# Performance work log

Measured on AMD Instinct MI355X. Metric: run time of the kernel, lower is better.

## Reference

```python
import jax, jax.numpy as jnp
import numpy as np

N_NODES = 50000
N_EDGES = 100000
N_GRAPHS = 2000
F_IN = 32      # num_node_features
EF = 16        # num_edge_features (unpacked bits)
H = 32         # hidden_dim
H2 = 64        # hidden_dim * 2


def _lin(key, fan_in, fan_out):
    kw, kb = jax.random.split(key)
    scale = 1.0 / np.sqrt(fan_in)
    W = jax.random.uniform(kw, (fan_in, fan_out), jnp.float32, -scale, scale)
    b = jax.random.uniform(kb, (fan_out,), jnp.float32, -scale, scale)
    return W, b


def setup_inputs() -> dict:
    key = jax.random.key(0)
    ks = jax.random.split(key, 16)
    x = jax.random.normal(ks[0], (N_NODES, F_IN), jnp.float32)
    edge_index = jax.random.randint(ks[1], (2, N_EDGES), 0, N_NODES, jnp.int64)
    edge_attr_packed = jax.random.randint(ks[2], (N_EDGES, 2), 0, 256, jnp.int32)
    batch = jnp.sort(jax.random.randint(ks[3], (N_NODES,), 0, N_GRAPHS, jnp.int64))

    W1a, b1a = _lin(ks[4], EF, H * F_IN)
    W1b, b1b = _lin(ks[5], H * F_IN, H * F_IN)
    W2a, b2a = _lin(ks[6], EF, H * H)
    W2b, b2b = _lin(ks[7], H * H, H * H * 2)
    root1 = jax.random.normal(ks[8], (F_IN, H), jnp.float32) / np.sqrt(F_IN)
    bias1 = jnp.zeros((H,), jnp.float32)
    root2 = jax.random.normal(ks[9], (H, H2), jnp.float32) / np.sqrt(H)
    bias2 = jnp.zeros((H2,), jnp.float32)
    fcW1, fcb1 = _lin(ks[10], H2, 512)
    fcW2, fcb2 = _lin(ks[11], 512, 512)
    fcW3, fcb3 = _lin(ks[12], 512, 256)
    fcW4, fcb4 = _lin(ks[13], 256, 3)
    return dict(x=x, edge_index=edge_index, edge_attr_packed=edge_attr_packed, batch=batch,
                W1a=W1a, b1a=b1a, W1b=W1b, b1b=b1b, W2a=W2a, b2a=b2a, W2b=W2b, b2b=b2b,
                root1=root1, bias1=bias1, root2=root2, bias2=bias2,
                fcW1=fcW1, fcb1=fcb1, fcW2=fcW2, fcb2=fcb2,
                fcW3=fcW3, fcb3=fcb3, fcW4=fcW4, fcb4=fcb4)


def _unpack_bits(ea_packed):
    # MSB-first bit unpack of each byte, matching torch f_unpackbits(mask=1)
    shifts = jnp.arange(7, -1, -1, dtype=jnp.int32)          # [8]
    bits = (ea_packed[:, :, None] >> shifts) & 1             # [E, W, 8]
    return bits.reshape(ea_packed.shape[0], -1).astype(jnp.float32)  # [E, W*8]


def _seg_mean(vals, idx, n):
    s = jax.ops.segment_sum(vals, idx, num_segments=n)
    c = jax.ops.segment_sum(jnp.ones((vals.shape[0], 1), vals.dtype), idx, num_segments=n)
    return s / jnp.maximum(c, 1.0)


def _nnconv(x, src, dst, theta, root, bias, f_in, f_out):
    # theta: [E, f_in*f_out] -> per-edge weight matrices (PyG view(-1, in, out))
    Wm = theta.reshape(-1, f_in, f_out)
    msg = jnp.einsum('ei,eio->eo', x[src], Wm)               # per-edge matmul
    agg = _seg_mean(msg, dst, x.shape[0])                    # scatter-mean at targets
    return agg + x @ root + bias


def reference(x, edge_index, edge_attr_packed, batch,
              W1a, b1a, W1b, b1b, W2a, b2a, W2b, b2b,
              root1, bias1, root2, bias2,
              fcW1, fcb1, fcW2, fcb2, fcW3, fcb3, fcW4, fcb4):
    relu = jax.nn.relu
    ea = _unpack_bits(edge_attr_packed)                      # [E, 16]
    src, dst = edge_index[0], edge_index[1]

    theta1 = relu(ea @ W1a + b1a) @ W1b + b1b                # [E, H*F_IN]
    h = relu(_nnconv(x, src, dst, theta1, root1, bias1, F_IN, H))

    theta2 = relu(ea @ W2a + b2a) @ W2b + b2b                # [E, H*H2]
    h = relu(_nnconv(h, src, dst, theta2, root2, bias2, H, H2))

    g = _seg_mean(h, batch, N_GRAPHS)                        # global_mean_pool
    g = relu(g @ fcW1 + fcb1)
    g = relu(g @ fcW2 + fcb2)
    g = relu(g @ fcW3 + fcb3)
    return g @ fcW4 + fcb4
```

## Files before the change

### kernel.cpp

```cpp
#include <hip/hip_runtime.h>

#define E_N 100000
#define NV_N 50000
#define NG_N 2000

typedef short s8v __attribute__((ext_vector_type(8)));
typedef unsigned short u16x8 __attribute__((ext_vector_type(8)));
typedef unsigned int u32x4 __attribute__((ext_vector_type(4)));
typedef float f32x4 __attribute__((ext_vector_type(4)));

__device__ __forceinline__ float bf2f(unsigned short u) {
  return __uint_as_float(((unsigned int)u) << 16);
}
__device__ __forceinline__ unsigned short f2bf(float f) {
  unsigned int u = __float_as_uint(f);
  u = u + 0x7fffu + ((u >> 16) & 1u);
  return (unsigned short)(u >> 16);
}


__global__ void k_tables(const float* __restrict__ W1a, const float* __restrict__ b1a,
                         const float* __restrict__ W2a, const float* __restrict__ b2a,
                         unsigned short* __restrict__ tabs) {
  int tid = blockIdx.x * 256 + threadIdx.x;
  int tb = tid >> 18, v = (tid >> 10) & 255, k = tid & 1023;
  const float* W = (tb < 2) ? W1a : W2a;
  int rbase = (tb & 1) ? 8 : 0;
  float s = 0.f;
  if ((tb & 1) == 0) s = (tb < 2) ? b1a[k] : b2a[k];
  #pragma unroll
  for (int j = 0; j < 8; ++j)
    if ((v >> (7 - j)) & 1) s += W[(rbase + j) * 1024 + k];
  tabs[tid] = f2bf(s);
}

__global__ void k_pack(const float* __restrict__ src, unsigned short* __restrict__ dst, int N) {
  int tid = blockIdx.x * 256 + threadIdx.x;
  int total = (1024 / 8) * N;
  if (tid >= total) return;
  int fi = tid >> 6, r = tid & 63;
  int lg = r >> 4, ll = r & 15;
  int nf = fi & 1, ks = (fi >> 1) & 3;
  int rest = fi >> 3;
  int nc32 = N / 32;
  int cb = rest % nc32, q = rest / nc32;
  int k0 = q * 128 + ks * 32 + lg * 8;
  int n = cb * 32 + nf * 16 + ll;
  u16x8 v;
  #pragma unroll
  for (int u = 0; u < 8; ++u)
    v[u] = f2bf(src[(size_t)(k0 + u) * N + n]);
  *(u16x8*)&dst[(size_t)tid * 8] = v;
}

__global__ void k_count(const int* __restrict__ ei, int* __restrict__ cnt) {
  int e = blockIdx.x * 256 + threadIdx.x;
  if (e < E_N) atomicAdd(&cnt[ei[E_N + e]], 1);
}

template<int NCOLS, int FOUT>
__global__ void __launch_bounds__(256, 2)
k_edge(const float* __restrict__ xsrc, const int* __restrict__ ei,
       const int* __restrict__ eap,
       const unsigned short* __restrict__ tab0,
       const unsigned short* __restrict__ tab1,
       const unsigned short* __restrict__ WP,
       const float* __restrict__ bvec,
       float* __restrict__ agg)
{
  constexpr int NP = NCOLS / 64;

  __shared__ unsigned short sHid[128 * 128];
  __shared__ float sXT[32 * 132];
  __shared__ int sSrc[128], sDst[128];
  __shared__ unsigned char sb0[128], sb1[128];

  const int t = threadIdx.x;
  const int l = t & 63;
  const int wid = t >> 6;
  const int wr = wid >> 1;
  const int wc = wid & 1;
  const int lg = l >> 4;
  const int ll = l & 15;
  const int e0 = blockIdx.x * 128;

  auto build = [&](int q) {
    int m = t >> 1, half = t & 1;
    const unsigned short* p0 = tab0 + (size_t)sb0[m] * 1024 + q * 128 + half * 64;
    const unsigned short* p1 = tab1 + (size_t)sb1[m] * 1024 + q * 128 + half * 64;
    #pragma unroll
    for (int j = 0; j < 8; ++j) {
      u16x8 a = *(const u16x8*)(p0 + j * 8);
      u16x8 b = *(const u16x8*)(p1 + j * 8);
      u32x4 hw;
      #pragma unroll
      for (int p = 0; p < 4; ++p) {
        float f0 = fmaxf(bf2f(a[2 * p]) + bf2f(b[2 * p]), 0.f);
        float f1 = fmaxf(bf2f(a[2 * p + 1]) + bf2f(b[2 * p + 1]), 0.f);
        unsigned int r01;
        asm("v_cvt_pk_bf16_f32 %0, %1, %2" : "=v"(r01) : "v"(f0), "v"(f1));
        hw[p] = r01;
      }
      int kb = half * 8 + j;
      *(u32x4*)&sHid[m * 128 + 8 * (kb ^ (m & 15))] = hw;
    }
  };

  const unsigned short* bp[4];
  #pragma unroll
  for (int k = 0; k < 4; ++k)
    bp[k] = WP + (size_t)((wc * 4 + k) * 2) * 512 + (size_t)l * 8;

  s8v rb[4][2];
  #pragma unroll
  for (int k = 0; k < 4; ++k) {
    rb[k][0] = *(const s8v*)bp[k];
    rb[k][1] = *(const s8v*)(bp[k] + 512);
    bp[k] += 8192;
  }

  if (t < 128) {
    int e = e0 + t;
    if (e < E_N) {
      sSrc[t] = ei[e]; sDst[t] = ei[E_N + e];
      sb0[t] = (unsigned char)(eap[2 * e] & 255);
      sb1[t] = (unsigned char)(eap[2 * e + 1] & 255);
    } else { sSrc[t] = 0; sDst[t] = -1; sb0[t] = 0; sb1[t] = 0; }
  }
  __syncthreads();
  for (int j = t; j < 128 * 32; j += 256) {
    int m = j >> 5, i = j & 31;
    sXT[i * 132 + m] = (e0 + m < E_N) ? xsrc[(size_t)sSrc[m] * 32 + i] : 0.f;
  }
  build(0);
  __syncthreads();

  f32x4 msgr[4][2] = {};

  #pragma unroll 1
  for (int q = 0; q < 8; ++q) {
    if (q > 0) {
      __syncthreads();
      build(q);
      __syncthreads();
    }
    s8v av[4][4];
    #pragma unroll
    for (int mf = 0; mf < 4; ++mf) {
      int row = wr * 64 + mf * 16 + ll;
      #pragma unroll
      for (int ks = 0; ks < 4; ++ks) {
        int kb = ks * 4 + lg;
        av[mf][ks] = *(const s8v*)&sHid[row * 128 + 8 * (kb ^ (row & 15))];
        asm volatile("" : "+v"(av[mf][ks]));
      }
    }
    #pragma unroll 1
    for (int np = 0; np < NP; ++np) {
      f32x4 acc[4][2];
      __builtin_amdgcn_s_setprio(1);
      #pragma unroll
      for (int mf = 0; mf < 4; ++mf)
        #pragma unroll
        for (int nf = 0; nf < 2; ++nf)
          acc[mf][nf] = __builtin_amdgcn_mfma_f32_16x16x32_bf16(
              av[mf][0], rb[0][nf], (f32x4){0.f, 0.f, 0.f, 0.f}, 0, 0, 0);
      __builtin_amdgcn_s_setprio(0);
      rb[0][0] = *(const s8v*)bp[0];
      rb[0][1] = *(const s8v*)(bp[0] + 512);
      bp[0] += 8192;
      __builtin_amdgcn_s_setprio(1);
      #pragma unroll
      for (int mf = 0; mf < 4; ++mf)
        #pragma unroll
        for (int nf = 0; nf < 2; ++nf)
          acc[mf][nf] = __builtin_amdgcn_mfma_f32_16x16x32_bf16(
              av[mf][1], rb[1][nf], acc[mf][nf], 0, 0, 0);
      __builtin_amdgcn_s_setprio(0);
      rb[1][0] = *(const s8v*)bp[1];
      rb[1][1] = *(const s8v*)(bp[1] + 512);
      bp[1] += 8192;
      __builtin_amdgcn_s_setprio(1);
      #pragma unroll
      for (int mf = 0; mf < 4; ++mf)
        #pragma unroll
        for (int nf = 0; nf < 2; ++nf)
          acc[mf][nf] = __builtin_amdgcn_mfma_f32_16x16x32_bf16(
              av[mf][2], rb[2][nf], acc[mf][nf], 0, 0, 0);
      __builtin_amdgcn_s_setprio(0);
      rb[2][0] = *(const s8v*)bp[2];
      rb[2][1] = *(const s8v*)(bp[2] + 512);
      bp[2] += 8192;
      __builtin_amdgcn_s_setprio(1);
      #pragma unroll
      for (int mf = 0; mf < 4; ++mf)
        #pragma unroll
        for (int nf = 0; nf < 2; ++nf)
          acc[mf][nf] = __builtin_amdgcn_mfma_f32_16x16x32_bf16(
              av[mf][3], rb[3][nf], acc[mf][nf], 0, 0, 0);
      __builtin_amdgcn_s_setprio(0);
      rb[3][0] = *(const s8v*)bp[3];
      rb[3][1] = *(const s8v*)(bp[3] + 512);
      bp[3] += 8192;

      const int iidx = (FOUT == 64) ? np : np * 2 + wc;
      #pragma unroll
      for (int mf = 0; mf < 4; ++mf) {
        f32x4 xv = *(const f32x4*)&sXT[iidx * 132 + wr * 64 + mf * 16 + lg * 4];
        msgr[mf][0] += acc[mf][0] * xv;
        msgr[mf][1] += acc[mf][1] * xv;
      }
    }
  }

  #pragma unroll 4
  for (int i = 0; i < 32; ++i) {
    if (FOUT == 32 && (i & 1) != wc) continue;
    float w0, w1;
    {
      int ob = (FOUT == 64) ? wc * 32 : 0;
      w0 = bvec[i * FOUT + ob + ll];
      w1 = bvec[i * FOUT + ob + 16 + ll];
    }
    #pragma unroll
    for (int mf = 0; mf < 4; ++mf) {
      f32x4 xv = *(const f32x4*)&sXT[i * 132 + wr * 64 + mf * 16 + lg * 4];
      msgr[mf][0] += xv * w0;
      msgr[mf][1] += xv * w1;
    }
  }

  #pragma unroll
  for (int nf = 0; nf < 2; ++nf) {
    const int o = ((FOUT == 64) ? (wc * 2 + nf) * 16 : nf * 16) + ll;
    #pragma unroll
    for (int mf = 0; mf < 4; ++mf)
      #pragma unroll
      for (int r = 0; r < 4; ++r) {
        int row = wr * 64 + mf * 16 + lg * 4 + r;
        int d = sDst[row];
        if (d >= 0) atomicAdd(&agg[(size_t)d * FOUT + o], msgr[mf][nf][r]);
      }
  }
}


__global__ void k_node1(const float* __restrict__ x, const float* __restrict__ agg,
                        const int* __restrict__ cnt, const float* __restrict__ root,
                        const float* __restrict__ bias, float* __restrict__ h) {
  int tid = blockIdx.x * 256 + threadIdx.x;
  if (tid >= NV_N * 32) return;
  int n = tid >> 5, j = tid & 31;
  const float* xr = x + n * 32;
  float s = 0.f;
  #pragma unroll
  for (int i = 0; i < 32; ++i) s = fmaf(xr[i], root[i * 32 + j], s);
  int c = cnt[n]; if (c < 1) c = 1;
  h[tid] = fmaxf(agg[tid] / (float)c + s + bias[j], 0.f);
}

__global__ void k_node2(const float* __restrict__ hin, const float* __restrict__ agg,
                        const int* __restrict__ cnt, const float* __restrict__ root,
                        const float* __restrict__ bias, float* __restrict__ h2) {
  int tid = blockIdx.x * 256 + threadIdx.x;
  if (tid >= NV_N * 64) return;
  int n = tid >> 6, j = tid & 63;
  const float* xr = hin + n * 32;
  float s = 0.f;
  #pragma unroll
  for (int i = 0; i < 32; ++i) s = fmaf(xr[i], root[i * 64 + j], s);
  int c = cnt[n]; if (c < 1) c = 1;
  h2[tid] = fmaxf(agg[tid] / (float)c + s + bias[j], 0.f);
}

__device__ __forceinline__ int lowerb(const int* __restrict__ a, int n, int key) {
  int lo = 0, hi = n;
  while (lo < hi) { int mid = (lo + hi) >> 1; if (a[mid] < key) lo = mid + 1; else hi = mid; }
  return lo;
}

__global__ void k_pool(const float* __restrict__ h2, const int* __restrict__ batch,
                       float* __restrict__ g) {
  int gid = (blockIdx.x * 256 + threadIdx.x) >> 6;
  int l = threadIdx.x & 63;
  if (gid >= NG_N) return;
  int lo = lowerb(batch, NV_N, gid);
  int hi = lowerb(batch, NV_N, gid + 1);
  float s = 0.f;
  for (int n = lo; n < hi; ++n) s += h2[n * 64 + l];
  int c = hi - lo; if (c < 1) c = 1;
  g[gid * 64 + l] = s / (float)c;
}

template<int K, bool RELU>
__global__ void k_fc(const float* __restrict__ A, const float* __restrict__ W,
                     const float* __restrict__ bias, float* __restrict__ out, int N) {
  __shared__ float sA[8][K];
  int r0 = blockIdx.x * 8;
  int n = blockIdx.y * 256 + threadIdx.x;
  for (int j = threadIdx.x; j < 8 * K; j += 256) {
    int rr = j / K, kk = j - rr * K;
    int r = r0 + rr;
    sA[rr][kk] = (r < NG_N) ? A[r * K + kk] : 0.f;
  }
  __syncthreads();
  float acc[8] = {0.f, 0.f, 0.f, 0.f, 0.f, 0.f, 0.f, 0.f};
  for (int k = 0; k < K; ++k) {
    float b = W[k * N + n];
    #pragma unroll
    for (int rr = 0; rr < 8; ++rr) acc[rr] = fmaf(sA[rr][k], b, acc[rr]);
  }
  float bs = bias[n];
  #pragma unroll
  for (int rr = 0; rr < 8; ++rr) {
    int r = r0 + rr;
    if (r < NG_N) {
      float v = acc[rr] + bs;
      if (RELU) v = fmaxf(v, 0.f);
      out[r * N + n] = v;
    }
  }
}

__global__ void k_fc4(const float* __restrict__ A, const float* __restrict__ W,
                      const float* __restrict__ bias, float* __restrict__ out) {
  int tid = blockIdx.x * 256 + threadIdx.x;
  int r = tid >> 2, s = tid & 3;
  if (r >= NG_N || s >= 3) return;
  float acc = bias[s];
  for (int k = 0; k < 256; ++k) acc = fmaf(A[r * 256 + k], W[k * 3 + s], acc);
  out[r * 3 + s] = acc;
}


extern "C" void kernel_launch(void* const* d_in, const int* in_sizes, int n_in,
                              void* d_out, int out_size, void* d_ws, size_t ws_size,
                              hipStream_t stream) {
  const float* x     = (const float*)d_in[0];
  const int*   ei    = (const int*)d_in[1];
  const int*   eap   = (const int*)d_in[2];
  const int*   batch = (const int*)d_in[3];
  const float* W1a   = (const float*)d_in[4];
  const float* b1a   = (const float*)d_in[5];
  const float* W1b   = (const float*)d_in[6];
  const float* b1b   = (const float*)d_in[7];
  const float* W2a   = (const float*)d_in[8];
  const float* b2a   = (const float*)d_in[9];
  const float* W2b   = (const float*)d_in[10];
  const float* b2b   = (const float*)d_in[11];
  const float* root1 = (const float*)d_in[12];
  const float* bias1 = (const float*)d_in[13];
  const float* root2 = (const float*)d_in[14];
  const float* bias2 = (const float*)d_in[15];
  const float* fcW1  = (const float*)d_in[16];
  const float* fcb1  = (const float*)d_in[17];
  const float* fcW2  = (const float*)d_in[18];
  const float* fcb2  = (const float*)d_in[19];
  const float* fcW3  = (const float*)d_in[20];
  const float* fcb3  = (const float*)d_in[21];
  const float* fcW4  = (const float*)d_in[22];
  const float* fcb4  = (const float*)d_in[23];
  float* out = (float*)d_out;

  char* w = (char*)d_ws;
  size_t off = 0;
  auto take = [&](size_t bytes) -> void* {
    void* p = w + off;
    off = (off + bytes + 255) & ~(size_t)255;
    return p;
  };
  unsigned short* tabs = (unsigned short*)take(4 * 256 * 1024 * 2);
  unsigned short* w1p  = (unsigned short*)take((size_t)1024 * 1024 * 2 + 32768);
  unsigned short* w2p  = (unsigned short*)take((size_t)1024 * 2048 * 2 + 32768);
  float* agg1 = (float*)take((size_t)NV_N * 32 * 4);
  float* agg2 = (float*)take((size_t)NV_N * 64 * 4);
  int*   cnt  = (int*)take((size_t)NV_N * 4);
  float* h    = (float*)take((size_t)NV_N * 32 * 4);
  float* h2   = (float*)take((size_t)NV_N * 64 * 4);
  float* g    = (float*)take((size_t)NG_N * 64 * 4);
  float* l1   = (float*)take((size_t)NG_N * 512 * 4);
  float* l2   = (float*)take((size_t)NG_N * 512 * 4);
  float* l3   = (float*)take((size_t)NG_N * 256 * 4);

  hipMemsetAsync(agg1, 0, (size_t)NV_N * 32 * 4, stream);
  hipMemsetAsync(agg2, 0, (size_t)NV_N * 64 * 4, stream);
  hipMemsetAsync(cnt, 0, (size_t)NV_N * 4, stream);

  k_tables<<<4096, 256, 0, stream>>>(W1a, b1a, W2a, b2a, tabs);
  k_pack<<<(1024 * 1024 / 8 + 255) / 256, 256, 0, stream>>>(W1b, w1p, 1024);
  k_pack<<<(1024 * 2048 / 8 + 255) / 256, 256, 0, stream>>>(W2b, w2p, 2048);
  k_count<<<(E_N + 255) / 256, 256, 0, stream>>>(ei, cnt);

  const int nblk = (E_N + 127) / 128;
  k_edge<1024, 32><<<nblk, 256, 0, stream>>>(x, ei, eap, tabs, tabs + 262144,
                                             w1p, b1b, agg1);
  k_node1<<<(NV_N * 32) / 256, 256, 0, stream>>>(x, agg1, cnt, root1, bias1, h);

  k_edge<2048, 64><<<nblk, 256, 0, stream>>>(h, ei, eap, tabs + 2 * 262144, tabs + 3 * 262144,
                                             w2p, b2b, agg2);
  k_node2<<<(NV_N * 64) / 256, 256, 0, stream>>>(h, agg2, cnt, root2, bias2, h2);

  k_pool<<<(NG_N * 64) / 256, 256, 0, stream>>>(h2, batch, g);

  k_fc<64, true><<<dim3((NG_N + 7) / 8, 2), 256, 0, stream>>>(g, fcW1, fcb1, l1, 512);
  k_fc<512, true><<<dim3((NG_N + 7) / 8, 2), 256, 0, stream>>>(l1, fcW2, fcb2, l2, 512);
  k_fc<512, true><<<dim3((NG_N + 7) / 8, 1), 256, 0, stream>>>(l2, fcW3, fcb3, l3, 256);
  k_fc4<<<(NG_N * 4 + 255) / 256, 256, 0, stream>>>(l3, fcW4, fcb4, out);
}
```

Baseline: 811.9 us.

## Pre-gather source features into transposed global buffer instead of per-block LDS staging

Adds a separate gather kernel that writes source-node features per edge into a transposed [32, EP] global array. The edge kernel then reads x values straight from global memory inside the MFMA loop instead of staging them in shared memory. This removes the sXT LDS buffer and the gather-with-sync prologue, which may improve occupancy. In exchange it adds two extra kernel launches, about 12.8 MB of write and read traffic, and global loads inside the inner loop.

```diff
diff --git a/kernel.cpp b/kernel.cpp
--- a/kernel.cpp
+++ b/kernel.cpp
@@ -3,6 +3,7 @@
 #define E_N 100000
 #define NV_N 50000
 #define NG_N 2000
+#define EP 100096
 
 typedef short s8v __attribute__((ext_vector_type(8)));
 typedef unsigned short u16x8 __attribute__((ext_vector_type(8)));
@@ -58,9 +59,24 @@
   if (e < E_N) atomicAdd(&cnt[ei[E_N + e]], 1);
 }
 
+__global__ void k_gat(const float* __restrict__ feat, const int* __restrict__ ei,
+                      float* __restrict__ xgT) {
+  int e = blockIdx.x * 256 + threadIdx.x;
+  if (e >= EP) return;
+  if (e < E_N) {
+    const float* fr = feat + (size_t)ei[e] * 32;
+    #pragma unroll
+    for (int i = 0; i < 32; ++i) xgT[(size_t)i * EP + e] = fr[i];
+  } else {
+    #pragma unroll
+    for (int i = 0; i < 32; ++i) xgT[(size_t)i * EP + e] = 0.f;
+  }
+}
+
 template<int NCOLS, int FOUT>
 __global__ void __launch_bounds__(256, 2)
-k_edge(const float* __restrict__ xsrc, const int* __restrict__ ei,
+k_edge(const float* __restrict__ xgT,
+       const int* __restrict__ ei,
        const int* __restrict__ eap,
        const unsigned short* __restrict__ tab0,
        const unsigned short* __restrict__ tab1,
@@ -71,8 +87,7 @@
   constexpr int NP = NCOLS / 64;
 
   __shared__ unsigned short sHid[128 * 128];
-  __shared__ float sXT[32 * 132];
-  __shared__ int sSrc[128], sDst[128];
+  __shared__ int sDst[128];
   __shared__ unsigned char sb0[128], sb1[128];
 
   const int t = threadIdx.x;
@@ -122,20 +137,17 @@
   if (t < 128) {
     int e = e0 + t;
     if (e < E_N) {
-      sSrc[t] = ei[e]; sDst[t] = ei[E_N + e];
+      sDst[t] = ei[E_N + e];
       sb0[t] = (unsigned char)(eap[2 * e] & 255);
       sb1[t] = (unsigned char)(eap[2 * e + 1] & 255);
-    } else { sSrc[t] = 0; sDst[t] = -1; sb0[t] = 0; sb1[t] = 0; }
+    } else { sDst[t] = -1; sb0[t] = 0; sb1[t] = 0; }
   }
   __syncthreads();
-  for (int j = t; j < 128 * 32; j += 256) {
-    int m = j >> 5, i = j & 31;
-    sXT[i * 132 + m] = (e0 + m < E_N) ? xsrc[(size_t)sSrc[m] * 32 + i] : 0.f;
-  }
   build(0);
   __syncthreads();
 
   f32x4 msgr[4][2] = {};
+  const float* xbase = xgT + e0 + wr * 64 + lg * 4;
 
   #pragma unroll 1
   for (int q = 0; q < 8; ++q) {
@@ -157,6 +169,13 @@
     }
     #pragma unroll 1
     for (int np = 0; np < NP; ++np) {
+      const int iidx = (FOUT == 64) ? np : np * 2 + wc;
+      f32x4 xv[4];
+      {
+        const float* px = xbase + (size_t)iidx * EP;
+        #pragma unroll
+        for (int mf = 0; mf < 4; ++mf) xv[mf] = *(const f32x4*)(px + mf * 16);
+      }
       f32x4 acc[4][2];
       __builtin_amdgcn_s_setprio(1);
       #pragma unroll
@@ -203,12 +222,10 @@
       rb[3][1] = *(const s8v*)(bp[3] + 512);
       bp[3] += 8192;
 
-      const int iidx = (FOUT == 64) ? np : np * 2 + wc;
       #pragma unroll
       for (int mf = 0; mf < 4; ++mf) {
-        f32x4 xv = *(const f32x4*)&sXT[iidx * 132 + wr * 64 + mf * 16 + lg * 4];
-        msgr[mf][0] += acc[mf][0] * xv;
-        msgr[mf][1] += acc[mf][1] * xv;
+        msgr[mf][0] += acc[mf][0] * xv[mf];
+        msgr[mf][1] += acc[mf][1] * xv[mf];
       }
     }
   }
@@ -224,7 +241,7 @@
     }
     #pragma unroll
     for (int mf = 0; mf < 4; ++mf) {
-      f32x4 xv = *(const f32x4*)&sXT[i * 132 + wr * 64 + mf * 16 + lg * 4];
+      f32x4 xv = *(const f32x4*)(xbase + (size_t)i * EP + mf * 16);
       msgr[mf][0] += xv * w0;
       msgr[mf][1] += xv * w1;
     }
@@ -372,6 +389,7 @@
   unsigned short* tabs = (unsigned short*)take(4 * 256 * 1024 * 2);
   unsigned short* w1p  = (unsigned short*)take((size_t)1024 * 1024 * 2 + 32768);
   unsigned short* w2p  = (unsigned short*)take((size_t)1024 * 2048 * 2 + 32768);
+  float* xgT  = (float*)take((size_t)32 * EP * 4);
   float* agg1 = (float*)take((size_t)NV_N * 32 * 4);
   float* agg2 = (float*)take((size_t)NV_N * 64 * 4);
   int*   cnt  = (int*)take((size_t)NV_N * 4);
@@ -391,12 +409,14 @@
   k_pack<<<(1024 * 2048 / 8 + 255) / 256, 256, 0, stream>>>(W2b, w2p, 2048);
   k_count<<<(E_N + 255) / 256, 256, 0, stream>>>(ei, cnt);
 
-  const int nblk = (E_N + 127) / 128;
-  k_edge<1024, 32><<<nblk, 256, 0, stream>>>(x, ei, eap, tabs, tabs + 262144,
+  const int nblk = EP / 128;
+  k_gat<<<EP / 256, 256, 0, stream>>>(x, ei, xgT);
+  k_edge<1024, 32><<<nblk, 256, 0, stream>>>(xgT, ei, eap, tabs, tabs + 262144,
                                              w1p, b1b, agg1);
   k_node1<<<(NV_N * 32) / 256, 256, 0, stream>>>(x, agg1, cnt, root1, bias1, h);
 
-  k_edge<2048, 64><<<nblk, 256, 0, stream>>>(h, ei, eap, tabs + 2 * 262144, tabs + 3 * 262144,
+  k_gat<<<EP / 256, 256, 0, stream>>>(h, ei, xgT);
+  k_edge<2048, 64><<<nblk, 256, 0, stream>>>(xgT, ei, eap, tabs + 2 * 262144, tabs + 3 * 262144,
                                              w2p, b2b, agg2);
   k_node2<<<(NV_N * 64) / 256, 256, 0, stream>>>(h, agg2, cnt, root2, bias2, h2);
 
```

New measurement: 915.5 us. 1.13x slower.

## Retile edge kernel to 256-edge blocks of 512 threads with 64-wide K chunks

Applied to the files above, without the earlier changes.

The edge kernel now processes 256 edges per block with 8 waves instead of 128 edges with 4, so each weight fragment loaded from global memory is reused across twice as many edges. The K dimension is split into 16 chunks of 64 instead of 8 of 128, which halves the shared hidden buffer per row and the register footprint for A and B fragments. The weight packing layout changes to match. This also hoists the x loads ahead of the MFMAs. The cost is more block-wide barriers per block and a higher occupancy target that may force register spills.

```diff
diff --git a/kernel.cpp b/kernel.cpp
--- a/kernel.cpp
+++ b/kernel.cpp
@@ -3,6 +3,7 @@
 #define E_N 100000
 #define NV_N 50000
 #define NG_N 2000
+#define EP 100096
 
 typedef short s8v __attribute__((ext_vector_type(8)));
 typedef unsigned short u16x8 __attribute__((ext_vector_type(8)));
@@ -40,11 +41,11 @@
   if (tid >= total) return;
   int fi = tid >> 6, r = tid & 63;
   int lg = r >> 4, ll = r & 15;
-  int nf = fi & 1, ks = (fi >> 1) & 3;
-  int rest = fi >> 3;
+  int nf = fi & 1, ks = (fi >> 1) & 1;
+  int rest = fi >> 2;
   int nc32 = N / 32;
   int cb = rest % nc32, q = rest / nc32;
-  int k0 = q * 128 + ks * 32 + lg * 8;
+  int k0 = q * 64 + ks * 32 + lg * 8;
   int n = cb * 32 + nf * 16 + ll;
   u16x8 v;
   #pragma unroll
@@ -59,7 +60,7 @@
 }
 
 template<int NCOLS, int FOUT>
-__global__ void __launch_bounds__(256, 2)
+__global__ void __launch_bounds__(512, 4)
 k_edge(const float* __restrict__ xsrc, const int* __restrict__ ei,
        const int* __restrict__ eap,
        const unsigned short* __restrict__ tab0,
@@ -70,10 +71,10 @@
 {
   constexpr int NP = NCOLS / 64;
 
-  __shared__ unsigned short sHid[128 * 128];
-  __shared__ float sXT[32 * 132];
-  __shared__ int sSrc[128], sDst[128];
-  __shared__ unsigned char sb0[128], sb1[128];
+  __shared__ unsigned short sHid[256 * 64];
+  __shared__ float sX[32 * 264];
+  __shared__ int sSrc[256], sDst[256];
+  __shared__ unsigned char sb0[256], sb1[256];
 
   const int t = threadIdx.x;
   const int l = t & 63;
@@ -82,14 +83,14 @@
   const int wc = wid & 1;
   const int lg = l >> 4;
   const int ll = l & 15;
-  const int e0 = blockIdx.x * 128;
+  const int e0 = blockIdx.x * 256;
 
   auto build = [&](int q) {
     int m = t >> 1, half = t & 1;
-    const unsigned short* p0 = tab0 + (size_t)sb0[m] * 1024 + q * 128 + half * 64;
-    const unsigned short* p1 = tab1 + (size_t)sb1[m] * 1024 + q * 128 + half * 64;
-    #pragma unroll
-    for (int j = 0; j < 8; ++j) {
+    const unsigned short* p0 = tab0 + (size_t)sb0[m] * 1024 + q * 64 + half * 32;
+    const unsigned short* p1 = tab1 + (size_t)sb1[m] * 1024 + q * 64 + half * 32;
+    #pragma unroll
+    for (int j = 0; j < 4; ++j) {
       u16x8 a = *(const u16x8*)(p0 + j * 8);
       u16x8 b = *(const u16x8*)(p1 + j * 8);
       u32x4 hw;
@@ -101,25 +102,20 @@
         asm("v_cvt_pk_bf16_f32 %0, %1, %2" : "=v"(r01) : "v"(f0), "v"(f1));
         hw[p] = r01;
       }
-      int kb = half * 8 + j;
-      *(u32x4*)&sHid[m * 128 + 8 * (kb ^ (m & 15))] = hw;
+      int kb = half * 4 + j;
+      *(u32x4*)&sHid[m * 64 + 8 * (kb ^ (m & 7))] = hw;
     }
   };
 
-  const unsigned short* bp[4];
-  #pragma unroll
-  for (int k = 0; k < 4; ++k)
-    bp[k] = WP + (size_t)((wc * 4 + k) * 2) * 512 + (size_t)l * 8;
-
-  s8v rb[4][2];
-  #pragma unroll
-  for (int k = 0; k < 4; ++k) {
-    rb[k][0] = *(const s8v*)bp[k];
-    rb[k][1] = *(const s8v*)(bp[k] + 512);
-    bp[k] += 8192;
-  }
-
-  if (t < 128) {
+  const unsigned short* bp = WP + (size_t)(4 * wc) * 512 + (size_t)l * 8;
+  s8v rb[2][2];
+  rb[0][0] = *(const s8v*)bp;
+  rb[0][1] = *(const s8v*)(bp + 512);
+  rb[1][0] = *(const s8v*)(bp + 1024);
+  rb[1][1] = *(const s8v*)(bp + 1536);
+  bp += 4096;
+
+  if (t < 256) {
     int e = e0 + t;
     if (e < E_N) {
       sSrc[t] = ei[e]; sDst[t] = ei[E_N + e];
@@ -128,9 +124,9 @@
     } else { sSrc[t] = 0; sDst[t] = -1; sb0[t] = 0; sb1[t] = 0; }
   }
   __syncthreads();
-  for (int j = t; j < 128 * 32; j += 256) {
+  for (int j = t; j < 256 * 32; j += 512) {
     int m = j >> 5, i = j & 31;
-    sXT[i * 132 + m] = (e0 + m < E_N) ? xsrc[(size_t)sSrc[m] * 32 + i] : 0.f;
+    sX[i * 264 + m] = (e0 + m < E_N) ? xsrc[(size_t)sSrc[m] * 32 + i] : 0.f;
   }
   build(0);
   __syncthreads();
@@ -138,25 +134,30 @@
   f32x4 msgr[4][2] = {};
 
   #pragma unroll 1
-  for (int q = 0; q < 8; ++q) {
+  for (int q = 0; q < 16; ++q) {
     if (q > 0) {
       __syncthreads();
       build(q);
       __syncthreads();
     }
-    s8v av[4][4];
+    s8v av[4][2];
     #pragma unroll
     for (int mf = 0; mf < 4; ++mf) {
       int row = wr * 64 + mf * 16 + ll;
       #pragma unroll
-      for (int ks = 0; ks < 4; ++ks) {
+      for (int ks = 0; ks < 2; ++ks) {
         int kb = ks * 4 + lg;
-        av[mf][ks] = *(const s8v*)&sHid[row * 128 + 8 * (kb ^ (row & 15))];
+        av[mf][ks] = *(const s8v*)&sHid[row * 64 + 8 * (kb ^ (row & 7))];
         asm volatile("" : "+v"(av[mf][ks]));
       }
     }
     #pragma unroll 1
     for (int np = 0; np < NP; ++np) {
+      const int iidx = (FOUT == 64) ? np : np * 2 + wc;
+      f32x4 xv[4];
+      #pragma unroll
+      for (int mf = 0; mf < 4; ++mf)
+        xv[mf] = *(const f32x4*)&sX[iidx * 264 + wr * 64 + mf * 16 + lg * 4];
       f32x4 acc[4][2];
       __builtin_amdgcn_s_setprio(1);
       #pragma unroll
@@ -166,9 +167,8 @@
           acc[mf][nf] = __builtin_amdgcn_mfma_f32_16x16x32_bf16(
               av[mf][0], rb[0][nf], (f32x4){0.f, 0.f, 0.f, 0.f}, 0, 0, 0);
       __builtin_amdgcn_s_setprio(0);
-      rb[0][0] = *(const s8v*)bp[0];
-      rb[0][1] = *(const s8v*)(bp[0] + 512);
-      bp[0] += 8192;
+      rb[0][0] = *(const s8v*)bp;
+      rb[0][1] = *(const s8v*)(bp + 512);
       __builtin_amdgcn_s_setprio(1);
       #pragma unroll
       for (int mf = 0; mf < 4; ++mf)
@@ -177,38 +177,14 @@
           acc[mf][nf] = __builtin_amdgcn_mfma_f32_16x16x32_bf16(
               av[mf][1], rb[1][nf], acc[mf][nf], 0, 0, 0);
       __builtin_amdgcn_s_setprio(0);
-      rb[1][0] = *(const s8v*)bp[1];
-      rb[1][1] = *(const s8v*)(bp[1] + 512);
-      bp[1] += 8192;
-      __builtin_amdgcn_s_setprio(1);
-      #pragma unroll
-      for (int mf = 0; mf < 4; ++mf)
-        #pragma unroll
-        for (int nf = 0; nf < 2; ++nf)
-          acc[mf][nf] = __builtin_amdgcn_mfma_f32_16x16x32_bf16(
-              av[mf][2], rb[2][nf], acc[mf][nf], 0, 0, 0);
-      __builtin_amdgcn_s_setprio(0);
-      rb[2][0] = *(const s8v*)bp[2];
-      rb[2][1] = *(const s8v*)(bp[2] + 512);
-      bp[2] += 8192;
-      __builtin_amdgcn_s_setprio(1);
-      #pragma unroll
-      for (int mf = 0; mf < 4; ++mf)
-        #pragma unroll
-        for (int nf = 0; nf < 2; ++nf)
-          acc[mf][nf] = __builtin_amdgcn_mfma_f32_16x16x32_bf16(
-              av[mf][3], rb[3][nf], acc[mf][nf], 0, 0, 0);
-      __builtin_amdgcn_s_setprio(0);
-      rb[3][0] = *(const s8v*)bp[3];
-      rb[3][1] = *(const s8v*)(bp[3] + 512);
-      bp[3] += 8192;
-
-      const int iidx = (FOUT == 64) ? np : np * 2 + wc;
+      rb[1][0] = *(const s8v*)(bp + 1024);
+      rb[1][1] = *(const s8v*)(bp + 1536);
+      bp += 4096;
+
       #pragma unroll
       for (int mf = 0; mf < 4; ++mf) {
-        f32x4 xv = *(const f32x4*)&sXT[iidx * 132 + wr * 64 + mf * 16 + lg * 4];
-        msgr[mf][0] += acc[mf][0] * xv;
-        msgr[mf][1] += acc[mf][1] * xv;
+        msgr[mf][0] += acc[mf][0] * xv[mf];
+        msgr[mf][1] += acc[mf][1] * xv[mf];
       }
     }
   }
@@ -224,7 +200,7 @@
     }
     #pragma unroll
     for (int mf = 0; mf < 4; ++mf) {
-      f32x4 xv = *(const f32x4*)&sXT[i * 132 + wr * 64 + mf * 16 + lg * 4];
+      f32x4 xv = *(const f32x4*)&sX[i * 264 + wr * 64 + mf * 16 + lg * 4];
       msgr[mf][0] += xv * w0;
       msgr[mf][1] += xv * w1;
     }
@@ -391,12 +367,12 @@
   k_pack<<<(1024 * 2048 / 8 + 255) / 256, 256, 0, stream>>>(W2b, w2p, 2048);
   k_count<<<(E_N + 255) / 256, 256, 0, stream>>>(ei, cnt);
 
-  const int nblk = (E_N + 127) / 128;
-  k_edge<1024, 32><<<nblk, 256, 0, stream>>>(x, ei, eap, tabs, tabs + 262144,
+  const int nblk = EP / 256;
+  k_edge<1024, 32><<<nblk, 512, 0, stream>>>(x, ei, eap, tabs, tabs + 262144,
                                              w1p, b1b, agg1);
   k_node1<<<(NV_N * 32) / 256, 256, 0, stream>>>(x, agg1, cnt, root1, bias1, h);
 
-  k_edge<2048, 64><<<nblk, 256, 0, stream>>>(h, ei, eap, tabs + 2 * 262144, tabs + 3 * 262144,
+  k_edge<2048, 64><<<nblk, 512, 0, stream>>>(h, ei, eap, tabs + 2 * 262144, tabs + 3 * 262144,
                                              w2p, b2b, agg2);
   k_node2<<<(NV_N * 64) / 256, 256, 0, stream>>>(h, agg2, cnt, root2, bias2, h2);
 
```

Result: slower. 1.711 ms (+110.8%).
